# Kernel tuning notes

Measured on AMD Instinct MI355X. Metric: run time of the kernel, lower is better.

The kernel has to match this reference:

```python
import jax, jax.numpy as jnp
import numpy as np

MIX_TIME = 20
NUM_SAMPLES = 128
NUM_ONES = 64


def setup_inputs() -> dict:
    key = jax.random.key(0)
    kz, ka, kw = jax.random.split(key, 3)
    B, D, DZ = 128, 512, 512
    z = (jax.random.uniform(kz, (B, DZ)) < 0.5).astype(jnp.float32)  # conditioned binary vars
    A = jax.random.normal(ka, (D, D), dtype=jnp.float32) * 0.02      # pairwise couplings
    W = jax.random.normal(kw, (D, DZ), dtype=jnp.float32) * 0.02     # w-z couplings
    return {"z": z, "A": A, "W": W}


def reference(z, A, W):
    # Batched conditional double-flip Gibbs sampler.
    # State x: (S, B, D) binary floats; per step pick distinct coords (i, j),
    # evaluate unnormalized log p(w|z) for the 4 value combos, sample categorically.
    S = NUM_SAMPLES
    B, DZ = z.shape
    D = A.shape[0]

    x0 = jnp.zeros((S, B, D), dtype=jnp.float32).at[..., :NUM_ONES].set(1.0)
    cond = jnp.broadcast_to(z[None], (S, B, DZ))  # (S,B,DZ)

    def logp(w):  # quadratic energy: w^T A w + w^T W z  -> (S,B)
        return (jnp.einsum('sbd,de,sbe->sb', w, A, w)
                + jnp.einsum('sbd,dk,sbk->sb', w, W, cond))

    combos = jnp.array([[0., 0.], [0., 1.], [1., 0.], [1., 1.]], dtype=jnp.float32)

    def step(x, k):
        ki, ks = jax.random.split(k)
        ij = jax.random.choice(ki, D, (2,), replace=False)  # distinct i, j
        i, j = ij[0], ij[1]

        def set_ij(v):  # clone x with coords (i,j) set to (v0, v1)
            return x.at[..., i].set(v[0]).at[..., j].set(v[1])

        xs = jax.vmap(set_ij)(combos)                    # (4,S,B,D)
        logits = jnp.moveaxis(jax.vmap(logp)(xs), 0, -1)  # (S,B,4)
        samp = jax.random.categorical(ks, logits)         # (S,B) in {0,1,2,3}
        iv = (samp // 2).astype(x.dtype)
        jv = (samp % 2).astype(x.dtype)
        x = x.at[..., i].set(iv).at[..., j].set(jv)
        return x, None

    keys = jax.random.split(jax.random.key(1), MIX_TIME)
    x, _ = jax.lax.scan(step, x0, keys)
    return x
```

## Files before the change

### kernel.cpp

```cpp
#include <hip/hip_runtime.h>
#include <stdint.h>

#define MIX_TIME 20
#define NCHAIN   16384
#define DDIM     512

#define WS_TBL 0
#define WS_SC  128
#define WS_T0  288
#define WS_U0  800
#define WS_ST0 1312
#define WS_SZ0 1344
#define WS_C   1472

struct U2 { uint32_t a, b; };

__device__ __forceinline__ uint32_t rotl32(uint32_t v, int r) {
  return (v << r) | (v >> (32 - r));
}

__device__ __forceinline__ U2 tf2x32(uint32_t k0, uint32_t k1, uint32_t x0, uint32_t x1) {
  const uint32_t ks2 = k0 ^ k1 ^ 0x1BD11BDAu;
  x0 += k0; x1 += k1;
  x0 += x1; x1 = rotl32(x1, 13); x1 ^= x0;
  x0 += x1; x1 = rotl32(x1, 15); x1 ^= x0;
  x0 += x1; x1 = rotl32(x1, 26); x1 ^= x0;
  x0 += x1; x1 = rotl32(x1,  6); x1 ^= x0;
  x0 += k1; x1 += ks2 + 1u;
  x0 += x1; x1 = rotl32(x1, 17); x1 ^= x0;
  x0 += x1; x1 = rotl32(x1, 29); x1 ^= x0;
  x0 += x1; x1 = rotl32(x1, 16); x1 ^= x0;
  x0 += x1; x1 = rotl32(x1, 24); x1 ^= x0;
  x0 += ks2; x1 += k0 + 2u;
  x0 += x1; x1 = rotl32(x1, 13); x1 ^= x0;
  x0 += x1; x1 = rotl32(x1, 15); x1 ^= x0;
  x0 += x1; x1 = rotl32(x1, 26); x1 ^= x0;
  x0 += x1; x1 = rotl32(x1,  6); x1 ^= x0;
  x0 += k0; x1 += k1 + 3u;
  x0 += x1; x1 = rotl32(x1, 17); x1 ^= x0;
  x0 += x1; x1 = rotl32(x1, 29); x1 ^= x0;
  x0 += x1; x1 = rotl32(x1, 16); x1 ^= x0;
  x0 += x1; x1 = rotl32(x1, 24); x1 ^= x0;
  x0 += k1; x1 += ks2 + 4u;
  x0 += x1; x1 = rotl32(x1, 13); x1 ^= x0;
  x0 += x1; x1 = rotl32(x1, 15); x1 ^= x0;
  x0 += x1; x1 = rotl32(x1, 26); x1 ^= x0;
  x0 += x1; x1 = rotl32(x1,  6); x1 ^= x0;
  x0 += ks2; x1 += k0 + 5u;
  return {x0, x1};
}

__device__ __forceinline__ uint32_t rbits32(uint32_t k0, uint32_t k1, uint32_t m) {
  U2 r = tf2x32(k0, k1, 0u, m);
  return r.a ^ r.b;
}
__device__ __forceinline__ U2 split_key(uint32_t k0, uint32_t k1, uint32_t idx) {
  return tf2x32(k0, k1, 0u, idx);
}

__device__ __forceinline__ float gumbel_from(uint32_t bits) {
  float u = __uint_as_float(0x3f800000u | (bits >> 9)) - 1.0f;
  u = fmaxf(u + 1.17549435e-38f, 1.17549435e-38f);
  return -logf(-logf(u));
}

__device__ __forceinline__ float bpermf(int byteidx, float v) {
  return __int_as_float(__builtin_amdgcn_ds_bpermute(byteidx, __float_as_int(v)));
}
__device__ __forceinline__ uint32_t bpermu(int byteidx, uint32_t v) {
  return (uint32_t)__builtin_amdgcn_ds_bpermute(byteidx, (int)v);
}

__global__ __launch_bounds__(256)
void pre_kernel(const float* __restrict__ A, const float* __restrict__ W,
                const float* __restrict__ z, uint32_t* __restrict__ wsu,
                float* __restrict__ wsf) {
  const int bid = blockIdx.x, tid = threadIdx.x;
  uint32_t* tbl = wsu + WS_TBL;
  uint32_t* sc  = wsu + WS_SC;
  float* T0  = wsf + WS_T0;
  float* U0  = wsf + WS_U0;
  float* St0 = wsf + WS_ST0;
  float* Sz0 = wsf + WS_SZ0;
  float* C   = wsf + WS_C;

  __shared__ float  sred[64];
  __shared__ float4 zs4[8][128];
  __shared__ float  credL[8][64];

  if (bid < MIX_TIME) {
    if (tid >= 64) return;
    const uint32_t t    = (uint32_t)bid;
    const uint32_t lane = (uint32_t)tid;
    const U2 K   = split_key(0u, 1u, t);
    const U2 ki  = split_key(K.a, K.b, 0u);
    const U2 ks  = split_key(K.a, K.b, 1u);
    const U2 sub = split_key(ki.a, ki.b, 1u);

    uint32_t k1 = 0xFFFFFFFFu, m1 = 0xFFFFFFFFu;
    uint32_t k2 = 0xFFFFFFFFu, m2 = 0xFFFFFFFFu;
    #pragma unroll
    for (int p = 0; p < 8; ++p) {
      const uint32_t m   = lane + 64u * (uint32_t)p;
      const uint32_t key = rbits32(sub.a, sub.b, m);
      const bool lt1 = (key < k1) || (key == k1 && m < m1);
      const bool lt2 = (key < k2) || (key == k2 && m < m2);
      if (lt1)      { k2 = k1; m2 = m1; k1 = key; m1 = m; }
      else if (lt2) { k2 = key; m2 = m; }
    }
    #pragma unroll
    for (int msk = 1; msk < 64; msk <<= 1) {
      const uint32_t ok1 = __shfl_xor((int)k1, msk, 64);
      const uint32_t om1 = __shfl_xor((int)m1, msk, 64);
      const uint32_t ok2 = __shfl_xor((int)k2, msk, 64);
      const uint32_t om2 = __shfl_xor((int)m2, msk, 64);
      const bool oless = (ok1 < k1) || (ok1 == k1 && om1 < m1);
      if (oless) {
        const bool l2 = (k1 < ok2) || (k1 == ok2 && m1 < om2);
        const uint32_t nk2 = l2 ? k1 : ok2, nm2 = l2 ? m1 : om2;
        k1 = ok1; m1 = om1; k2 = nk2; m2 = nm2;
      } else {
        const bool l2 = (ok1 < k2) || (ok1 == k2 && om1 < m2);
        if (l2) { k2 = ok1; m2 = om1; }
      }
    }
    if (lane == 0) {
      tbl[4u * t + 0u] = m1;
      tbl[4u * t + 1u] = m2;
      tbl[4u * t + 2u] = ks.a;
      tbl[4u * t + 3u] = ks.b;
      sc[8u * t + 0u] = m1;
      sc[8u * t + 1u] = m2;
      sc[8u * t + 6u] = 0u;
      sc[8u * t + 7u] = 0u;
    }
    if (lane < 4) {
      const uint32_t r = (lane < 2) ? m1 : m2;
      const uint32_t c = (lane & 1) ? m2 : m1;
      sc[8u * t + 2u + lane] = __float_as_uint(A[(size_t)r * DDIM + c]);
    }
    return;
  }

  if (bid <= MIX_TIME + 1) {
    const int e = (bid - MIX_TIME) * 256 + tid;
    float s = 0.f;
    #pragma unroll 1
    for (int d = 0; d < 64; ++d) s += A[(size_t)d * DDIM + e];
    T0[e] = s;
    if (bid == MIX_TIME) {
      if (tid < 64) sred[tid] = s;
      __syncthreads();
      if (tid == 0) {
        float q = 0.f;
        #pragma unroll 1
        for (int e2 = 0; e2 < 64; ++e2) q += sred[e2];
        St0[0] = q;
      }
    }
    return;
  }

  if (bid <= MIX_TIME + 3) {
    const int d = (bid - MIX_TIME - 2) * 256 + tid;
    const float4* Ar = reinterpret_cast<const float4*>(A + (size_t)d * DDIM);
    float s = 0.f;
    #pragma unroll
    for (int k = 0; k < 16; ++k) {
      const float4 v = Ar[k];
      s += v.x; s += v.y; s += v.z; s += v.w;
    }
    U0[d] = s;
    return;
  }

  const int cb = bid - (MIX_TIME + 4);
  const int bg = cb >> 3, slab = cb & 7;
  #pragma unroll
  for (int k = 0; k < 4; ++k) {
    const int idx = tid + 256 * k;
    const int br = idx >> 7, c4i = idx & 127;
    zs4[br][c4i] = reinterpret_cast<const float4*>(z + (size_t)(bg * 8 + br) * DDIM)[c4i];
  }
  __syncthreads();
  const int r = tid & 63;
  const int h = tid >> 6;
  const int d = slab * 64 + r;
  const float4* Wr = reinterpret_cast<const float4*>(W + (size_t)d * DDIM);
  float s0 = 0.f, s1 = 0.f;
  #pragma unroll 4
  for (int k = 0; k < 128; ++k) {
    const float4 w = Wr[k];
    const float4 za = zs4[2 * h][k], zb = zs4[2 * h + 1][k];
    s0 = fmaf(w.x, za.x, s0); s0 = fmaf(w.y, za.y, s0);
    s0 = fmaf(w.z, za.z, s0); s0 = fmaf(w.w, za.w, s0);
    s1 = fmaf(w.x, zb.x, s1); s1 = fmaf(w.y, zb.y, s1);
    s1 = fmaf(w.z, zb.z, s1); s1 = fmaf(w.w, zb.w, s1);
  }
  C[(size_t)(bg * 8 + 2 * h) * DDIM + d]     = s0;
  C[(size_t)(bg * 8 + 2 * h + 1) * DDIM + d] = s1;
  if (slab == 0) { credL[2 * h][r] = s0; credL[2 * h + 1][r] = s1; }
  __syncthreads();
  if (slab == 0 && tid < 8) {
    float s = 0.f;
    #pragma unroll 1
    for (int e = 0; e < 64; ++e) s += credL[tid][e];
    Sz0[bg * 8 + tid] = s;
  }
}

__global__ __launch_bounds__(256)
void gibbs8_kernel(const float* __restrict__ A,
                   const uint32_t* __restrict__ wsu,
                   const float* __restrict__ wsf,
                   float* __restrict__ out) {
  const int tid = threadIdx.x;
  const int l = tid & 63, wv = tid >> 6;
  const uint32_t* tbl = wsu + WS_TBL;
  const uint32_t* sc  = wsu + WS_SC;
  const float* T0w  = wsf + WS_T0;
  const float* U0w  = wsf + WS_U0;
  const float* St0w = wsf + WS_ST0;
  const float* Sz0w = wsf + WS_SZ0;
  const float* Cw   = wsf + WS_C;

  __shared__ __align__(16) float gg[3200];
  __shared__ uint32_t tblL[80];
  if (tid < 80) tblL[tid] = tbl[tid];
  __syncthreads();
  #pragma unroll 1
  for (int p = tid; p < 1600; p += 256) {
    const int r = p / 40, c = p % 40;
    const uint32_t cr = tblL[4 * (r >> 1) + (r & 1)];
    const uint32_t cc = tblL[4 * (c >> 1) + (c & 1)];
    gg[p]        = A[(size_t)cr * DDIM + cc];
    gg[1600 + p] = A[(size_t)cc * DDIM + cr];
  }

  const int ql  = l >> 3;
  const int seg = l & 7;
  const uint32_t chainbase = ((uint32_t)blockIdx.x * 4u + (uint32_t)wv) * 8u;
  const uint32_t chain_l = chainbase + (uint32_t)ql;
  const uint32_t b_l = chain_l & 127u;

  float fTi[3], fTj[3], fUi[3], fUj[3], fci[3], fcj[3], fxi[3], fxj[3];
  uint32_t iiK[3], jjK[3];
  const float* ggb[3];
  #pragma unroll
  for (int k = 0; k < 3; ++k) {
    const int tp = 8 * k + seg;
    const int tc = (tp < MIX_TIME) ? tp : 0;
    const uint32_t i = sc[8 * tc], j = sc[8 * tc + 1];
    iiK[k] = i; jjK[k] = j;
    fTi[k] = T0w[i];  fTj[k] = T0w[j];
    fUi[k] = U0w[i];  fUj[k] = U0w[j];
    fci[k] = Cw[(size_t)b_l * DDIM + i];
    fcj[k] = Cw[(size_t)b_l * DDIM + j];
    fxi[k] = (i < 64u) ? 1.f : 0.f;
    fxj[k] = (j < 64u) ? 1.f : 0.f;
    ggb[k] = &gg[2 * tc];
  }
  float St = St0w[0];
  float Sz = Sz0w[b_l];
  uint32_t mlo = (seg == 0) ? 0xFFFFFFFFu : 0u;
  uint32_t mhi = mlo;

  float garr[10];
  #pragma unroll
  for (int k = 0; k < 10; ++k) {
    const int f = 64 * k + l;
    const int t = f >> 5;
    const uint32_t qg = ((uint32_t)l & 31u) >> 2;
    const uint32_t m  = (chainbase + qg) * 4u + (uint32_t)(l & 3);
    garr[k] = gumbel_from(rbits32(tbl[4 * t + 2], tbl[4 * t + 3], m));
  }
  __syncthreads();

  #pragma unroll
  for (int t = 0; t < MIX_TIME; ++t) {
    const int kS = t >> 3;
    const int bidx = ((l & 0x38) + (t & 7)) << 2;
    const float Ti  = bpermf(bidx, fTi[kS]);
    const float Tj  = bpermf(bidx, fTj[kS]);
    const float Ui  = bpermf(bidx, fUi[kS]);
    const float Uj  = bpermf(bidx, fUj[kS]);
    const float cib = bpermf(bidx, fci[kS]);
    const float cjb = bpermf(bidx, fcj[kS]);
    const float xi  = bpermf(bidx, fxi[kS]);
    const float xj  = bpermf(bidx, fxj[kS]);
    const int gq = ((t & 1) << 7) + (ql << 4);
    const float gv0 = bpermf(gq + 0,  garr[t >> 1]);
    const float gv1 = bpermf(gq + 4,  garr[t >> 1]);
    const float gv2 = bpermf(gq + 8,  garr[t >> 1]);
    const float gv3 = bpermf(gq + 12, garr[t >> 1]);

    const uint32_t ii = sc[8 * t], jj = sc[8 * t + 1];
    const float Aii = __uint_as_float(sc[8 * t + 2]);
    const float Aij = __uint_as_float(sc[8 * t + 3]);
    const float Aji = __uint_as_float(sc[8 * t + 4]);
    const float Ajj = __uint_as_float(sc[8 * t + 5]);

    const float si   = Ui - xi * Aii - xj * Aij;
    const float sj   = Uj - xi * Aji - xj * Ajj;
    const float sTR  = St - xi * Ti - xj * Tj;
    const float szR  = Sz - xi * cib - xj * cjb;
    const float QR   = sTR - xi * si - xj * sj;
    const float coli = Ti - xi * Aii - xj * Aji;
    const float colj = Tj - xi * Aij - xj * Ajj;
    const float base = QR + szR;
    const float gi   = si + coli + Aii + cib;
    const float gj   = sj + colj + Ajj + cjb;
    const float gij  = Aij + Aji;

    const float v0 = gv0 + base;
    const float v1 = gv1 + (base + gj);
    const float v2 = gv2 + (base + gi);
    const float v3 = gv3 + (base + gi + gj + gij);

    int bestc = 0; float bv = v0;
    if (v1 > bv) { bv = v1; bestc = 1; }
    if (v2 > bv) { bv = v2; bestc = 2; }
    if (v3 > bv) { bv = v3; bestc = 3; }

    const int ian = (bestc >> 1) & 1, ibn = bestc & 1;
    const float fan = (float)ian, fbn = (float)ibn;
    const float fdi = fan - xi, fdj = fbn - xj;

    St = St + fdi * Ti + fdj * Tj
            + fdi * (si + fan * Aii + fbn * Aij)
            + fdj * (sj + fan * Aji + fbn * Ajj);
    Sz = Sz + fdi * cib + fdj * cjb;

    #pragma unroll
    for (int k = 0; k < 3; ++k) {
      if (t < 8 * k + 7) {
        const float2 ga = *reinterpret_cast<const float2*>(ggb[k] + 80 * t);
        const float2 gB = *reinterpret_cast<const float2*>(ggb[k] + 80 * t + 40);
        const float2 gc = *reinterpret_cast<const float2*>(ggb[k] + 1600 + 80 * t);
        const float2 gd = *reinterpret_cast<const float2*>(ggb[k] + 1600 + 80 * t + 40);
        fTi[k] = fmaf(fdi, ga.x, fmaf(fdj, gB.x, fTi[k]));
        fTj[k] = fmaf(fdi, ga.y, fmaf(fdj, gB.y, fTj[k]));
        fUi[k] = fmaf(fdi, gc.x, fmaf(fdj, gd.x, fUi[k]));
        fUj[k] = fmaf(fdi, gc.y, fmaf(fdj, gd.y, fUj[k]));
        fxi[k] = (iiK[k] == ii) ? fan : fxi[k];
        fxi[k] = (iiK[k] == jj) ? fbn : fxi[k];
        fxj[k] = (jjK[k] == ii) ? fan : fxj[k];
        fxj[k] = (jjK[k] == jj) ? fbn : fxj[k];
      }
    }

    {
      const uint32_t ib = 1u << (ii & 31u);
      const uint32_t nv = (uint32_t)(-(int)ian) & ib;
      const bool own_i = ((uint32_t)seg == (ii >> 6));
      if ((ii >> 5) & 1u) { if (own_i) mhi = (mhi & ~ib) | nv; }
      else                { if (own_i) mlo = (mlo & ~ib) | nv; }
      const uint32_t jb = 1u << (jj & 31u);
      const uint32_t nj = (uint32_t)(-(int)ibn) & jb;
      const bool own_j = ((uint32_t)seg == (jj >> 6));
      if ((jj >> 5) & 1u) { if (own_j) mhi = (mhi & ~jb) | nj; }
      else                { if (own_j) mlo = (mlo & ~jb) | nj; }
    }
  }

  {
    float* wavebase = out + (size_t)chainbase * DDIM;
    #pragma unroll
    for (int g = 0; g < 16; ++g) {
      const int bidx = 16 * g + ((l >> 4) << 2);
      const uint32_t wlo = bpermu(bidx, mlo);
      const uint32_t whi = bpermu(bidx, mhi);
      const uint32_t w   = ((l >> 3) & 1) ? whi : wlo;
      const uint32_t nib = (w >> (4 * (l & 7))) & 0xFu;
      float4 o;
      o.x = (float)( nib       & 1u);
      o.y = (float)((nib >> 1) & 1u);
      o.z = (float)((nib >> 2) & 1u);
      o.w = (float)((nib >> 3) & 1u);
      *reinterpret_cast<float4*>(
          wavebase + (size_t)((g >> 1) * 512 + (64 * (g & 1) + l) * 4)) = o;
    }
  }
}

extern "C" void kernel_launch(void* const* d_in, const int* in_sizes, int n_in,
                              void* d_out, int out_size, void* d_ws, size_t ws_size,
                              hipStream_t stream) {
  const float* z = (const float*)d_in[0];
  const float* A = (const float*)d_in[1];
  const float* W = (const float*)d_in[2];
  float* out = (float*)d_out;
  uint32_t* wsu = (uint32_t*)d_ws;
  float*    wsf = (float*)d_ws;

  hipLaunchKernelGGL(pre_kernel, dim3(MIX_TIME + 4 + 128), dim3(256), 0, stream,
                     A, W, z, wsu, wsf);
  hipLaunchKernelGGL(gibbs8_kernel, dim3(NCHAIN / 32), dim3(256), 0, stream,
                     A, wsu, wsf, out);
}
```

Measured before the change: 49.20 us.

## Compute each step's categorical choice in one owner lane and broadcast a packed result

The old loop broadcast eight per-step operands and four Gumbel values to every lane with ds_bpermute each step. Now the lane whose segment owns step t evaluates the step using its own registers. Each lane precomputes its own Gumbel noise for the steps it owns, and one packed integer holding the deltas and choice is broadcast, along with St and Sz, at the start of the next step. This cuts cross-lane permute traffic from about twelve to three per step. In exchange the state updates are deferred by one step, which adds a serial dependency between consecutive steps and a final epilogue for the last step.

```diff
diff --git a/kernel.cpp b/kernel.cpp
--- a/kernel.cpp
+++ b/kernel.cpp
@@ -264,37 +264,72 @@
   float Sz = Sz0w[b_l];
   uint32_t mlo = (seg == 0) ? 0xFFFFFFFFu : 0u;
   uint32_t mhi = mlo;
-
-  float garr[10];
+  int pk = 0;
+
+  float g2[3][4];
   #pragma unroll
-  for (int k = 0; k < 10; ++k) {
-    const int f = 64 * k + l;
-    const int t = f >> 5;
-    const uint32_t qg = ((uint32_t)l & 31u) >> 2;
-    const uint32_t m  = (chainbase + qg) * 4u + (uint32_t)(l & 3);
-    garr[k] = gumbel_from(rbits32(tbl[4 * t + 2], tbl[4 * t + 3], m));
+  for (int k = 0; k < 3; ++k) {
+    const int tp = 8 * k + seg;
+    const int tc = (tp < MIX_TIME) ? tp : 0;
+    const uint32_t k0g = tbl[4 * tc + 2], k1g = tbl[4 * tc + 3];
+    #pragma unroll
+    for (int c = 0; c < 4; ++c)
+      g2[k][c] = gumbel_from(rbits32(k0g, k1g, chain_l * 4u + (uint32_t)c));
   }
   __syncthreads();
 
   #pragma unroll
   for (int t = 0; t < MIX_TIME; ++t) {
+    if (t > 0) {
+      const int s = t - 1;
+      const int srcb = ((l & 0x38) + (s & 7)) << 2;
+      const int   pks = __builtin_amdgcn_ds_bpermute(srcb, pk);
+      const float StP = bpermf(srcb, St);
+      const float SzP = bpermf(srcb, Sz);
+      St = StP; Sz = SzP;
+      const float fdi_s = (float)((pks & 3) - 1);
+      const float fdj_s = (float)(((pks >> 2) & 3) - 1);
+      const int ian_s = (pks >> 5) & 1, ibn_s = (pks >> 4) & 1;
+      const float fan_s = (float)ian_s, fbn_s = (float)ibn_s;
+      const uint32_t iiP = sc[8 * s], jjP = sc[8 * s + 1];
+
+      #pragma unroll
+      for (int k = 0; k < 3; ++k) {
+        if (s < 8 * k + 7) {
+          const float2 ga = *reinterpret_cast<const float2*>(ggb[k] + 80 * s);
+          const float2 gB = *reinterpret_cast<const float2*>(ggb[k] + 80 * s + 40);
+          const float2 gc = *reinterpret_cast<const float2*>(ggb[k] + 1600 + 80 * s);
+          const float2 gd = *reinterpret_cast<const float2*>(ggb[k] + 1600 + 80 * s + 40);
+          fTi[k] = fmaf(fdi_s, ga.x, fmaf(fdj_s, gB.x, fTi[k]));
+          fTj[k] = fmaf(fdi_s, ga.y, fmaf(fdj_s, gB.y, fTj[k]));
+          fUi[k] = fmaf(fdi_s, gc.x, fmaf(fdj_s, gd.x, fUi[k]));
+          fUj[k] = fmaf(fdi_s, gc.y, fmaf(fdj_s, gd.y, fUj[k]));
+          fxi[k] = (iiK[k] == iiP) ? fan_s : fxi[k];
+          fxi[k] = (iiK[k] == jjP) ? fbn_s : fxi[k];
+          fxj[k] = (jjK[k] == iiP) ? fan_s : fxj[k];
+          fxj[k] = (jjK[k] == jjP) ? fbn_s : fxj[k];
+        }
+      }
+      {
+        const uint32_t ib = 1u << (iiP & 31u);
+        const uint32_t nv = (uint32_t)(-ian_s) & ib;
+        const bool own_i = ((uint32_t)seg == (iiP >> 6));
+        if ((iiP >> 5) & 1u) { if (own_i) mhi = (mhi & ~ib) | nv; }
+        else                 { if (own_i) mlo = (mlo & ~ib) | nv; }
+        const uint32_t jb = 1u << (jjP & 31u);
+        const uint32_t nj = (uint32_t)(-ibn_s) & jb;
+        const bool own_j = ((uint32_t)seg == (jjP >> 6));
+        if ((jjP >> 5) & 1u) { if (own_j) mhi = (mhi & ~jb) | nj; }
+        else                 { if (own_j) mlo = (mlo & ~jb) | nj; }
+      }
+    }
+
     const int kS = t >> 3;
-    const int bidx = ((l & 0x38) + (t & 7)) << 2;
-    const float Ti  = bpermf(bidx, fTi[kS]);
-    const float Tj  = bpermf(bidx, fTj[kS]);
-    const float Ui  = bpermf(bidx, fUi[kS]);
-    const float Uj  = bpermf(bidx, fUj[kS]);
-    const float cib = bpermf(bidx, fci[kS]);
-    const float cjb = bpermf(bidx, fcj[kS]);
-    const float xi  = bpermf(bidx, fxi[kS]);
-    const float xj  = bpermf(bidx, fxj[kS]);
-    const int gq = ((t & 1) << 7) + (ql << 4);
-    const float gv0 = bpermf(gq + 0,  garr[t >> 1]);
-    const float gv1 = bpermf(gq + 4,  garr[t >> 1]);
-    const float gv2 = bpermf(gq + 8,  garr[t >> 1]);
-    const float gv3 = bpermf(gq + 12, garr[t >> 1]);
-
-    const uint32_t ii = sc[8 * t], jj = sc[8 * t + 1];
+    const float Ti  = fTi[kS], Tj  = fTj[kS];
+    const float Ui  = fUi[kS], Uj  = fUj[kS];
+    const float cib = fci[kS], cjb = fcj[kS];
+    const float xi  = fxi[kS], xj  = fxj[kS];
+
     const float Aii = __uint_as_float(sc[8 * t + 2]);
     const float Aij = __uint_as_float(sc[8 * t + 3]);
     const float Aji = __uint_as_float(sc[8 * t + 4]);
@@ -312,10 +347,10 @@
     const float gj   = sj + colj + Ajj + cjb;
     const float gij  = Aij + Aji;
 
-    const float v0 = gv0 + base;
-    const float v1 = gv1 + (base + gj);
-    const float v2 = gv2 + (base + gi);
-    const float v3 = gv3 + (base + gi + gj + gij);
+    const float v0 = g2[kS][0] + base;
+    const float v1 = g2[kS][1] + (base + gj);
+    const float v2 = g2[kS][2] + (base + gi);
+    const float v3 = g2[kS][3] + (base + gi + gj + gij);
 
     int bestc = 0; float bv = v0;
     if (v1 > bv) { bv = v1; bestc = 1; }
@@ -331,36 +366,25 @@
             + fdj * (sj + fan * Aji + fbn * Ajj);
     Sz = Sz + fdi * cib + fdj * cjb;
 
-    #pragma unroll
-    for (int k = 0; k < 3; ++k) {
-      if (t < 8 * k + 7) {
-        const float2 ga = *reinterpret_cast<const float2*>(ggb[k] + 80 * t);
-        const float2 gB = *reinterpret_cast<const float2*>(ggb[k] + 80 * t + 40);
-        const float2 gc = *reinterpret_cast<const float2*>(ggb[k] + 1600 + 80 * t);
-        const float2 gd = *reinterpret_cast<const float2*>(ggb[k] + 1600 + 80 * t + 40);
-        fTi[k] = fmaf(fdi, ga.x, fmaf(fdj, gB.x, fTi[k]));
-        fTj[k] = fmaf(fdi, ga.y, fmaf(fdj, gB.y, fTj[k]));
-        fUi[k] = fmaf(fdi, gc.x, fmaf(fdj, gd.x, fUi[k]));
-        fUj[k] = fmaf(fdi, gc.y, fmaf(fdj, gd.y, fUj[k]));
-        fxi[k] = (iiK[k] == ii) ? fan : fxi[k];
-        fxi[k] = (iiK[k] == jj) ? fbn : fxi[k];
-        fxj[k] = (jjK[k] == ii) ? fan : fxj[k];
-        fxj[k] = (jjK[k] == jj) ? fbn : fxj[k];
-      }
-    }
-
-    {
-      const uint32_t ib = 1u << (ii & 31u);
-      const uint32_t nv = (uint32_t)(-(int)ian) & ib;
-      const bool own_i = ((uint32_t)seg == (ii >> 6));
-      if ((ii >> 5) & 1u) { if (own_i) mhi = (mhi & ~ib) | nv; }
-      else                { if (own_i) mlo = (mlo & ~ib) | nv; }
-      const uint32_t jb = 1u << (jj & 31u);
-      const uint32_t nj = (uint32_t)(-(int)ibn) & jb;
-      const bool own_j = ((uint32_t)seg == (jj >> 6));
-      if ((jj >> 5) & 1u) { if (own_j) mhi = (mhi & ~jb) | nj; }
-      else                { if (own_j) mlo = (mlo & ~jb) | nj; }
-    }
+    pk = ((int)fdi + 1) | (((int)fdj + 1) << 2) | (bestc << 4);
+  }
+
+  {
+    const int s = MIX_TIME - 1;
+    const int srcb = ((l & 0x38) + (s & 7)) << 2;
+    const int pks = __builtin_amdgcn_ds_bpermute(srcb, pk);
+    const int ian_s = (pks >> 5) & 1, ibn_s = (pks >> 4) & 1;
+    const uint32_t iiP = sc[8 * s], jjP = sc[8 * s + 1];
+    const uint32_t ib = 1u << (iiP & 31u);
+    const uint32_t nv = (uint32_t)(-ian_s) & ib;
+    const bool own_i = ((uint32_t)seg == (iiP >> 6));
+    if ((iiP >> 5) & 1u) { if (own_i) mhi = (mhi & ~ib) | nv; }
+    else                 { if (own_i) mlo = (mlo & ~ib) | nv; }
+    const uint32_t jb = 1u << (jjP & 31u);
+    const uint32_t nj = (uint32_t)(-ibn_s) & jb;
+    const bool own_j = ((uint32_t)seg == (jjP >> 6));
+    if ((jjP >> 5) & 1u) { if (own_j) mhi = (mhi & ~jb) | nj; }
+    else                 { if (own_j) mlo = (mlo & ~jb) | nj; }
   }
 
   {
```

New measurement: 48.64 us. No clear change (-1.1%).
